# Kernel optimization log

Measured on AMD Instinct MI355X. Metric: run time of the kernel, lower is better.

The kernel has to match this reference:

```python
import jax, jax.numpy as jnp
import numpy as np

N = 10000
F_IN = 512
HID = 256
N_CLS = 64


def setup_inputs() -> dict:
    key = jax.random.key(0)
    k_feat, k_adj, k_w1, k_b1, k_w2, k_b2 = jax.random.split(key, 6)
    feature = jax.random.normal(k_feat, (N, F_IN), dtype=jnp.float32)
    # normalized-adjacency-like dense matrix (sparse-ish values, scaled)
    adj = jax.random.uniform(k_adj, (N, N), dtype=jnp.float32) * (1.0 / N)
    # GCNConv params: glorot-style weights, zero bias
    s1 = 1.0 / np.sqrt(F_IN)
    s2 = 1.0 / np.sqrt(HID)
    W1 = jax.random.uniform(k_w1, (F_IN, HID), jnp.float32, -s1, s1)
    b1 = jnp.zeros((HID,), jnp.float32)
    W2 = jax.random.uniform(k_w2, (HID, N_CLS), jnp.float32, -s2, s2)
    b2 = jnp.zeros((N_CLS,), jnp.float32)
    return {"feature": feature, "adj": adj, "W1": W1, "b1": b1, "W2": W2, "b2": b2}


def gcn_conv(x, adj, W, b):
    # support = x @ W ; out = adj @ support + b
    return adj @ (x @ W) + b


def reference(feature, adj, W1, b1, W2, b2):
    x1 = jax.nn.relu(gcn_conv(feature, adj, W1, b1))
    # dropout is identity in eval mode
    x2 = gcn_conv(x1, adj, W2, b2)
    return (x1, jax.nn.log_softmax(x2, axis=1))
```

## Files before the change

kernel.cpp:

```cpp
#include <hip/hip_runtime.h>
#include <hip/hip_bf16.h>


#define NROW 10000
#define FIN  512
#define HID  256
#define NCLS 64
#define KP   10048
#define KSPLIT2 4
#define KSPAN2  2560
#define KSPLIT4 8
#define KSPAN4  1280

typedef __bf16 bf8_t __attribute__((ext_vector_type(8)));
typedef __bf16 bf4_t __attribute__((ext_vector_type(4)));
typedef float  f4_t  __attribute__((ext_vector_type(4)));

typedef __attribute__((address_space(3))) void       lds_void;
typedef const __attribute__((address_space(1))) void glb_void;

__device__ __forceinline__ void dma16(const void* g, void* l) {
    __builtin_amdgcn_global_load_lds((glb_void*)g, (lds_void*)l, 16, 0, 0);
}

__global__ void cvt_f32_bf16(const float* __restrict__ in, __bf16* __restrict__ out, int n) {
    int stride = gridDim.x * blockDim.x * 4;
    for (int i = (blockIdx.x * blockDim.x + threadIdx.x) * 4; i < n; i += stride) {
        f4_t v = *(const f4_t*)(in + i);
        bf4_t o;
        o[0] = (__bf16)v[0]; o[1] = (__bf16)v[1]; o[2] = (__bf16)v[2]; o[3] = (__bf16)v[3];
        *(bf4_t*)(out + i) = o;
    }
}

__global__ void cvt_adj_bf16(const float* __restrict__ adj, __bf16* __restrict__ adjb) {
    const int r = blockIdx.x;
    const float* src = adj + (long)r * NROW;
    __bf16* dst = adjb + (long)r * KP;
    for (int ch = threadIdx.x; ch < KP / 8; ch += 256) {
        bf8_t o;
        if (r < NROW && ch < NROW / 8) {
            f4_t a = *(const f4_t*)(src + ch * 8);
            f4_t b = *(const f4_t*)(src + ch * 8 + 4);
            o[0] = (__bf16)a[0]; o[1] = (__bf16)a[1]; o[2] = (__bf16)a[2]; o[3] = (__bf16)a[3];
            o[4] = (__bf16)b[0]; o[5] = (__bf16)b[1]; o[6] = (__bf16)b[2]; o[7] = (__bf16)b[3];
        } else {
            o = bf8_t{(__bf16)0.f, (__bf16)0.f, (__bf16)0.f, (__bf16)0.f,
                      (__bf16)0.f, (__bf16)0.f, (__bf16)0.f, (__bf16)0.f};
        }
        *(bf8_t*)(dst + ch * 8) = o;
    }
}

__global__ void cvt_transpose(const float* __restrict__ in, __bf16* __restrict__ out, int K, int Nn) {
    int idx = blockIdx.x * 256 + threadIdx.x;
    if (idx < K * Nn) {
        int k = idx / Nn, n = idx % Nn;
        out[n * K + k] = (__bf16)in[idx];
    }
}

template<int BN, int EPI>
__global__ void __launch_bounds__(256, (BN >= 256) ? 3 : 4)
gemm_bt(const __bf16* __restrict__ Ab, const __bf16* __restrict__ Bt,
        int M, int Nn, int K, int lda, int ldb, int kspan,
        float* __restrict__ outF, __bf16* __restrict__ outB,
        int ldo, long partStride)
{
    constexpr int BM = 64, BK = 64;
    constexpr int WM = BM / 2, WN = BN / 2;
    constexpr int MI = WM / 16, NI = WN / 16;
    constexpr int BCALLS = BN / 32;
    constexpr int ACALLS = BM / 32;
    __shared__ __bf16 As[BM * BK];
    __shared__ __bf16 Bs[BN * BK];

    const int tid  = threadIdx.x;
    const int lane = tid & 63;
    const int wave = tid >> 6;
    const int wm = wave >> 1, wn = wave & 1;
    const int m0 = blockIdx.x * BM;
    const int n0 = blockIdx.y * BN;
    const int kbase = blockIdx.z * kspan;
    const int kend  = min(K, kbase + kspan);

    f4_t acc[MI][NI];
    #pragma unroll
    for (int i = 0; i < MI; i++)
        #pragma unroll
        for (int j = 0; j < NI; j++)
            acc[i][j] = f4_t{0.f, 0.f, 0.f, 0.f};

    const int lrow  = lane & 15;
    const int koff0 = (lane >> 4) * 8;

    const __bf16* Brow[BCALLS];
    #pragma unroll
    for (int j = 0; j < BCALLS; ++j) {
        int c = wave + j * 4;
        Brow[j] = Bt + (long)(n0 + c * 8 + (lane >> 3)) * ldb + (lane & 7) * 8;
    }
    const __bf16* Arow[ACALLS];
    #pragma unroll
    for (int j = 0; j < ACALLS; ++j) {
        int c = wave + j * 4;
        Arow[j] = Ab + (long)(m0 + c * 8 + (lane >> 3)) * lda + (lane & 7) * 8;
    }

    for (int k0 = kbase; k0 < kend; k0 += BK) {
        #pragma unroll
        for (int j = 0; j < ACALLS; ++j)
            dma16(Arow[j] + k0, &As[(wave + j * 4) * 512]);
        #pragma unroll
        for (int j = 0; j < BCALLS; ++j)
            dma16(Brow[j] + k0, &Bs[(wave + j * 4) * 512]);

        __syncthreads();

        #pragma unroll
        for (int ks = 0; ks < BK; ks += 32) {
            bf8_t af[MI], bfv[NI];
            #pragma unroll
            for (int mi = 0; mi < MI; mi++)
                af[mi] = *(const bf8_t*)&As[(wm * WM + mi * 16 + lrow) * BK + ks + koff0];
            #pragma unroll
            for (int ni = 0; ni < NI; ni++)
                bfv[ni] = *(const bf8_t*)&Bs[(wn * WN + ni * 16 + lrow) * BK + ks + koff0];
            #pragma unroll
            for (int mi = 0; mi < MI; mi++)
                #pragma unroll
                for (int ni = 0; ni < NI; ni++)
                    acc[mi][ni] = __builtin_amdgcn_mfma_f32_16x16x32_bf16(
                        af[mi], bfv[ni], acc[mi][ni], 0, 0, 0);
        }
        __syncthreads();
    }

    const int erow = wm * WM + (lane >> 4) * 4;
    const int ecol = wn * WN + lrow;
    #pragma unroll
    for (int mi = 0; mi < MI; mi++) {
        #pragma unroll
        for (int ni = 0; ni < NI; ni++) {
            #pragma unroll
            for (int r = 0; r < 4; r++) {
                int grow = m0 + erow + mi * 16 + r;
                int gcol = n0 + ecol + ni * 16;
                if (grow < M && gcol < Nn) {
                    float v = acc[mi][ni][r];
                    if constexpr (EPI == 0) {
                        outB[(long)grow * ldo + gcol] = (__bf16)v;
                    } else {
                        outF[blockIdx.z * partStride + (long)grow * ldo + gcol] = v;
                    }
                }
            }
        }
    }
}

__global__ void relu_bias_fin(const float* __restrict__ part, const float* __restrict__ b1,
                              float* __restrict__ outF, __bf16* __restrict__ outB) {
    long i = (long)(blockIdx.x * 256 + threadIdx.x) * 4;
    f4_t v = *(const f4_t*)(part + i);
    #pragma unroll
    for (int s = 1; s < KSPLIT2; s++) {
        f4_t p = *(const f4_t*)(part + (long)s * NROW * HID + i);
        v[0] += p[0]; v[1] += p[1]; v[2] += p[2]; v[3] += p[3];
    }
    int col = (int)(i & (HID - 1));
    f4_t b = *(const f4_t*)(b1 + col);
    f4_t y;
    bf4_t yb;
    #pragma unroll
    for (int j = 0; j < 4; j++) {
        y[j] = fmaxf(v[j] + b[j], 0.f);
        yb[j] = (__bf16)y[j];
    }
    *(f4_t*)(outF + i) = y;
    *(bf4_t*)(outB + i) = yb;
}

__global__ void logsoftmax_fin(const float* __restrict__ part, const float* __restrict__ b2,
                               float* __restrict__ out, int M) {
    int row  = blockIdx.x * 4 + (threadIdx.x >> 6);
    int lane = threadIdx.x & 63;
    if (row >= M) return;
    float v = b2[lane];
    #pragma unroll
    for (int s = 0; s < KSPLIT4; s++) v += part[((long)s * M + row) * NCLS + lane];
    float m = v;
    #pragma unroll
    for (int off = 32; off > 0; off >>= 1) m = fmaxf(m, __shfl_xor(m, off));
    float e = __expf(v - m);
    float sum = e;
    #pragma unroll
    for (int off = 32; off > 0; off >>= 1) sum += __shfl_xor(sum, off);
    out[(long)row * NCLS + lane] = (v - m) - __logf(sum);
}

extern "C" void kernel_launch(void* const* d_in, const int* in_sizes, int n_in,
                              void* d_out, int out_size, void* d_ws, size_t ws_size,
                              hipStream_t stream) {
    const float* feat = (const float*)d_in[0];
    const float* adj  = (const float*)d_in[1];
    const float* W1   = (const float*)d_in[2];
    const float* b1   = (const float*)d_in[3];
    const float* W2   = (const float*)d_in[4];
    const float* b2   = (const float*)d_in[5];
    float* out = (float*)d_out;
    char* ws = (char*)d_ws;

    __bf16* featb = (__bf16*)(ws);
    __bf16* W1t   = (__bf16*)(ws + 10289152);
    __bf16* W2t   = (__bf16*)(ws + 10551296);
    __bf16* S1t   = (__bf16*)(ws + 10584064);
    __bf16* x1b   = (__bf16*)(ws + 15728640);
    __bf16* S2t   = (__bf16*)(ws + 20873216);
    float*  part  = (float*) (ws + 22159360);
    __bf16* adjb  = (__bf16*)(ws + 63119360);

    hipMemsetAsync(S1t, 0, (size_t)HID * KP * 2, stream);
    hipMemsetAsync(S2t, 0, (size_t)NCLS * KP * 2, stream);

    cvt_f32_bf16<<<640, 256, 0, stream>>>(feat, featb, NROW * FIN);
    cvt_adj_bf16<<<KP, 256, 0, stream>>>(adj, adjb);
    cvt_transpose<<<(FIN * HID + 255) / 256, 256, 0, stream>>>(W1, W1t, FIN, HID);
    cvt_transpose<<<(HID * NCLS + 255) / 256, 256, 0, stream>>>(W2, W2t, HID, NCLS);

    gemm_bt<64, 0><<<dim3(4, 157, 1), 256, 0, stream>>>(
        W1t, featb, HID, NROW, FIN, FIN, FIN, FIN,
        nullptr, S1t, KP, 0);

    gemm_bt<256, 2><<<dim3(157, 1, KSPLIT2), 256, 0, stream>>>(
        adjb, S1t, NROW, HID, KP, KP, KP, KSPAN2,
        part, nullptr, HID, (long)NROW * HID);

    relu_bias_fin<<<NROW * HID / 4 / 256, 256, 0, stream>>>(part, b1, out, x1b);

    gemm_bt<64, 0><<<dim3(1, 157, 1), 256, 0, stream>>>(
        W2t, x1b, NCLS, NROW, HID, HID, HID, HID,
        nullptr, S2t, KP, 0);

    gemm_bt<64, 2><<<dim3(157, 1, KSPLIT4), 256, 0, stream>>>(
        adjb, S2t, NROW, NCLS, KP, KP, KP, KSPAN4,
        part, nullptr, NCLS, (long)NROW * NCLS);

    logsoftmax_fin<<<2500, 256, 0, stream>>>(part, b2, out + (long)NROW * HID, NROW);
}
```

Measured before the change: 760.5 us.

## Swizzle bf16 operand layouts, double-buffer GEMM LDS loads, split adj GEMM N-tile

Stores every bf16 operand matrix (features, adjacency, transposed weights, intermediates) with an XOR swizzle of 8-element chunks within each 64-column group. The GEMM's LDS fragment reads undo the swizzle, which is meant to avoid LDS bank conflicts. The GEMM now double-buffers its global-to-LDS DMA so the next K tile loads while the current one computes, at the cost of twice the LDS. The first adjacency GEMM drops from BN=256 to BN=128 with two N blocks, which doubles parallelism but reads adjacency twice.

```diff
diff --git a/kernel.cpp b/kernel.cpp
--- a/kernel.cpp
+++ b/kernel.cpp
@@ -23,13 +23,19 @@
     __builtin_amdgcn_global_load_lds((glb_void*)g, (lds_void*)l, 16, 0, 0);
 }
 
-__global__ void cvt_f32_bf16(const float* __restrict__ in, __bf16* __restrict__ out, int n) {
+__device__ __forceinline__ int swzc(int k, int r) {
+    return (k & ~63) | ((((k >> 3) & 7) ^ (r & 7)) << 3) | (k & 7);
+}
+
+template<int LDW>
+__global__ void cvt_f32_bf16_swz(const float* __restrict__ in, __bf16* __restrict__ out, int n) {
     int stride = gridDim.x * blockDim.x * 4;
     for (int i = (blockIdx.x * blockDim.x + threadIdx.x) * 4; i < n; i += stride) {
         f4_t v = *(const f4_t*)(in + i);
         bf4_t o;
         o[0] = (__bf16)v[0]; o[1] = (__bf16)v[1]; o[2] = (__bf16)v[2]; o[3] = (__bf16)v[3];
-        *(bf4_t*)(out + i) = o;
+        int row = i / LDW, k = i & (LDW - 1);
+        *(bf4_t*)(out + (long)row * LDW + swzc(k, row)) = o;
     }
 }
 
@@ -48,7 +54,8 @@
             o = bf8_t{(__bf16)0.f, (__bf16)0.f, (__bf16)0.f, (__bf16)0.f,
                       (__bf16)0.f, (__bf16)0.f, (__bf16)0.f, (__bf16)0.f};
         }
-        *(bf8_t*)(dst + ch * 8) = o;
+        int swch = (ch & ~7) | ((ch & 7) ^ (r & 7));
+        *(bf8_t*)(dst + swch * 8) = o;
     }
 }
 
@@ -56,12 +63,12 @@
     int idx = blockIdx.x * 256 + threadIdx.x;
     if (idx < K * Nn) {
         int k = idx / Nn, n = idx % Nn;
-        out[n * K + k] = (__bf16)in[idx];
+        out[(long)n * K + swzc(k, n)] = (__bf16)in[idx];
     }
 }
 
 template<int BN, int EPI>
-__global__ void __launch_bounds__(256, (BN >= 256) ? 3 : 4)
+__global__ void __launch_bounds__(256, (BN >= 128) ? 3 : 4)
 gemm_bt(const __bf16* __restrict__ Ab, const __bf16* __restrict__ Bt,
         int M, int Nn, int K, int lda, int ldb, int kspan,
         float* __restrict__ outF, __bf16* __restrict__ outB,
@@ -70,10 +77,11 @@
     constexpr int BM = 64, BK = 64;
     constexpr int WM = BM / 2, WN = BN / 2;
     constexpr int MI = WM / 16, NI = WN / 16;
+    constexpr int ACALLS = BM / 32;
     constexpr int BCALLS = BN / 32;
-    constexpr int ACALLS = BM / 32;
-    __shared__ __bf16 As[BM * BK];
-    __shared__ __bf16 Bs[BN * BK];
+    constexpr int ASZ = BM * BK, BSZ = BN * BK;
+    __shared__ __bf16 As[2 * ASZ];
+    __shared__ __bf16 Bs[2 * BSZ];
 
     const int tid  = threadIdx.x;
     const int lane = tid & 63;
@@ -93,39 +101,54 @@
 
     const int lrow  = lane & 15;
     const int koff0 = (lane >> 4) * 8;
-
+    const int l7    = lrow & 7;
+
+    const __bf16* Arow[ACALLS];
+    #pragma unroll
+    for (int j = 0; j < ACALLS; ++j) {
+        int c = wave + j * 4;
+        Arow[j] = Ab + (long)(m0 + c * 8 + (lane >> 3)) * lda + (lane & 7) * 8;
+    }
     const __bf16* Brow[BCALLS];
     #pragma unroll
     for (int j = 0; j < BCALLS; ++j) {
         int c = wave + j * 4;
         Brow[j] = Bt + (long)(n0 + c * 8 + (lane >> 3)) * ldb + (lane & 7) * 8;
     }
-    const __bf16* Arow[ACALLS];
-    #pragma unroll
-    for (int j = 0; j < ACALLS; ++j) {
-        int c = wave + j * 4;
-        Arow[j] = Ab + (long)(m0 + c * 8 + (lane >> 3)) * lda + (lane & 7) * 8;
-    }
+
+    int cur = 0;
+    {
+        #pragma unroll
+        for (int j = 0; j < ACALLS; ++j)
+            dma16(Arow[j] + kbase, &As[(wave + j * 4) * 512]);
+        #pragma unroll
+        for (int j = 0; j < BCALLS; ++j)
+            dma16(Brow[j] + kbase, &Bs[(wave + j * 4) * 512]);
+    }
+    __syncthreads();
 
     for (int k0 = kbase; k0 < kend; k0 += BK) {
-        #pragma unroll
-        for (int j = 0; j < ACALLS; ++j)
-            dma16(Arow[j] + k0, &As[(wave + j * 4) * 512]);
-        #pragma unroll
-        for (int j = 0; j < BCALLS; ++j)
-            dma16(Brow[j] + k0, &Bs[(wave + j * 4) * 512]);
-
-        __syncthreads();
+        if (k0 + BK < kend) {
+            int nxt = cur ^ 1;
+            #pragma unroll
+            for (int j = 0; j < ACALLS; ++j)
+                dma16(Arow[j] + (k0 + BK), &As[nxt * ASZ + (wave + j * 4) * 512]);
+            #pragma unroll
+            for (int j = 0; j < BCALLS; ++j)
+                dma16(Brow[j] + (k0 + BK), &Bs[nxt * BSZ + (wave + j * 4) * 512]);
+        }
 
         #pragma unroll
         for (int ks = 0; ks < BK; ks += 32) {
+            const int cc = (ks + koff0) >> 3;
+            const int co = ((cc ^ l7) << 3);
             bf8_t af[MI], bfv[NI];
             #pragma unroll
             for (int mi = 0; mi < MI; mi++)
-                af[mi] = *(const bf8_t*)&As[(wm * WM + mi * 16 + lrow) * BK + ks + koff0];
+                af[mi] = *(const bf8_t*)&As[cur * ASZ + (wm * WM + mi * 16 + lrow) * BK + co];
             #pragma unroll
             for (int ni = 0; ni < NI; ni++)
-                bfv[ni] = *(const bf8_t*)&Bs[(wn * WN + ni * 16 + lrow) * BK + ks + koff0];
+                bfv[ni] = *(const bf8_t*)&Bs[cur * BSZ + (wn * WN + ni * 16 + lrow) * BK + co];
             #pragma unroll
             for (int mi = 0; mi < MI; mi++)
                 #pragma unroll
@@ -134,6 +157,7 @@
                         af[mi], bfv[ni], acc[mi][ni], 0, 0, 0);
         }
         __syncthreads();
+        cur ^= 1;
     }
 
     const int erow = wm * WM + (lane >> 4) * 4;
@@ -149,7 +173,7 @@
                 if (grow < M && gcol < Nn) {
                     float v = acc[mi][ni][r];
                     if constexpr (EPI == 0) {
-                        outB[(long)grow * ldo + gcol] = (__bf16)v;
+                        outB[(long)grow * ldo + swzc(gcol, grow)] = (__bf16)v;
                     } else {
                         outF[blockIdx.z * partStride + (long)grow * ldo + gcol] = v;
                     }
@@ -168,6 +192,7 @@
         f4_t p = *(const f4_t*)(part + (long)s * NROW * HID + i);
         v[0] += p[0]; v[1] += p[1]; v[2] += p[2]; v[3] += p[3];
     }
+    int row = (int)(i >> 8);
     int col = (int)(i & (HID - 1));
     f4_t b = *(const f4_t*)(b1 + col);
     f4_t y;
@@ -178,7 +203,7 @@
         yb[j] = (__bf16)y[j];
     }
     *(f4_t*)(outF + i) = y;
-    *(bf4_t*)(outB + i) = yb;
+    *(bf4_t*)(outB + (long)row * HID + swzc(col, row)) = yb;
 }
 
 __global__ void logsoftmax_fin(const float* __restrict__ part, const float* __restrict__ b2,
@@ -223,7 +248,7 @@
     hipMemsetAsync(S1t, 0, (size_t)HID * KP * 2, stream);
     hipMemsetAsync(S2t, 0, (size_t)NCLS * KP * 2, stream);
 
-    cvt_f32_bf16<<<640, 256, 0, stream>>>(feat, featb, NROW * FIN);
+    cvt_f32_bf16_swz<FIN><<<640, 256, 0, stream>>>(feat, featb, NROW * FIN);
     cvt_adj_bf16<<<KP, 256, 0, stream>>>(adj, adjb);
     cvt_transpose<<<(FIN * HID + 255) / 256, 256, 0, stream>>>(W1, W1t, FIN, HID);
     cvt_transpose<<<(HID * NCLS + 255) / 256, 256, 0, stream>>>(W2, W2t, HID, NCLS);
@@ -232,7 +257,7 @@
         W1t, featb, HID, NROW, FIN, FIN, FIN, FIN,
         nullptr, S1t, KP, 0);
 
-    gemm_bt<256, 2><<<dim3(157, 1, KSPLIT2), 256, 0, stream>>>(
+    gemm_bt<128, 2><<<dim3(157, 2, KSPLIT2), 256, 0, stream>>>(
         adjb, S1t, NROW, HID, KP, KP, KP, KSPAN2,
         part, nullptr, HID, (long)NROW * HID);
 
```

Measured after the change: 761.1 us. No clear change (+0.1%).
